# Kernel tuning notes

Hardware: AMD Instinct MI355X
Metric: run time of the kernel (lower is better)

The kernel has to match this reference:

```python
import jax, jax.numpy as jnp
import numpy as np

B, S, D_IN, H, BLOCKS, OUT_DIM = 32, 128, 16, 128, 3, 1
TAU = 0.5
BN_EPS = 1e-5


def _conv1d(x, w, b, dil):
    # x: [B, C, S], w: [O, I, K], 'same' padding with dilation (matches torch padding='same')
    y = jax.lax.conv_general_dilated(x, w, (1,), 'SAME', rhs_dilation=(dil,),
                                     dimension_numbers=('NCH', 'OIH', 'NCH'))
    return y + b[None, :, None]


def setup_inputs() -> dict:
    key = jax.random.key(0)
    ks = jax.random.split(key, 24)
    w = lambda k, shape, s=0.05: (jax.random.normal(k, shape, jnp.float32) * s)
    return {
        'data': jax.random.normal(ks[0], (B, S, D_IN), jnp.float32),
        'gumbel_u': jax.random.uniform(ks[1], (B, S * S, 2), jnp.float32),
        'w11': w(ks[2], (H, D_IN, 1)), 'b11': jnp.zeros((H,), jnp.float32),
        'w12': w(ks[3], (H, H, 3)),    'b12': jnp.zeros((H,), jnp.float32),
        'w21': w(ks[4], (H, D_IN, 1)), 'b21': jnp.zeros((H,), jnp.float32),
        'w22': w(ks[5], (H, H, 5)),    'b22': jnp.zeros((H,), jnp.float32),
        'w31': w(ks[6], (H, D_IN, 1)), 'b31': jnp.zeros((H,), jnp.float32),
        'wf': w(ks[7], (3 * H, H)),    'bf': jnp.zeros((H,), jnp.float32),
        'w1': w(ks[8], (2 * H, H)),    'b1': jnp.zeros((H,), jnp.float32),
        'w2': w(ks[9], (H, 2)),        'b2': jnp.zeros((2,), jnp.float32),
        'wl': w(ks[10], (BLOCKS, H, H)), 'bl': jnp.zeros((BLOCKS, H), jnp.float32),
        'wr': w(ks[11], (BLOCKS, H, H)),
        'gamma': jnp.ones((BLOCKS, H), jnp.float32), 'beta': jnp.zeros((BLOCKS, H), jnp.float32),
        'wg': w(ks[12], (BLOCKS, 1), 0.3), 'bg': jnp.zeros((1,), jnp.float32),
        'we': w(ks[13], (H, H // 2)),  'be': jnp.zeros((H // 2,), jnp.float32),
        'wo': w(ks[14], (H // 2, OUT_DIM)), 'bo': jnp.zeros((OUT_DIM,), jnp.float32),
    }


def reference(data, gumbel_u, w11, b11, w12, b12, w21, b21, w22, b22, w31, b31,
              wf, bf, w1, b1, w2, b2, wl, bl, wr, gamma, beta, wg, bg, we, be, wo, bo):
    b_, s_, _ = data.shape
    xd = jnp.transpose(data, (0, 2, 1))                    # [B, D_IN, S]
    # dilated TCN feature extraction
    x1 = _conv1d(_conv1d(xd, w11, b11, 1), w12, b12, 3)
    x2 = _conv1d(_conv1d(xd, w21, b21, 1), w22, b22, 5)
    x3 = _conv1d(xd, w31, b31, 1)
    x = jnp.concatenate([x1, x2, x3], axis=1)              # [B, 3H, S]
    x = jnp.transpose(x, (0, 2, 1))                        # [B, S, 3H]
    x = jax.nn.relu(x @ wf + bf)                           # [B, S, H] node features

    # edge scoring: pair (i,j) gets cat(sender=x[j], receiver=x[i]); fc1 split avoids [B,S,S,2H]
    hs = x @ w1[:H]                                        # sender part  [B, S, H]
    hr = x @ w1[H:]                                        # receiver part [B, S, H]
    h = jax.nn.relu(hs[:, None, :, :] + hr[:, :, None, :] + b1)  # [B, S(i), S(j), H]
    logits = h @ w2 + b2                                   # [B, S, S, 2]

    # hard gumbel-softmax, channel 0 = edge on
    u = jnp.clip(gumbel_u, 1e-6, 1.0 - 1e-6).reshape(b_, s_, s_, 2)
    g = -jnp.log(-jnp.log(u))
    y = (logits + g) / TAU
    adj = (jnp.argmax(y, axis=-1) == 0).astype(x.dtype)    # [B, S, S]
    # zero strict lower triangle (tri_mask) and diagonal (keep_self_loops=False)
    idx = jnp.arange(s_)
    adj = adj * (idx[None, :] > idx[:, None])[None]
    # edge_list in torch is non-differentiable -> no grad through adjacency
    adj = jax.lax.stop_gradient(adj)

    # SAGEConv (mean aggr) + BatchNorm, dense per-sample message passing
    deg = jnp.maximum(adj.sum(axis=1), 1.0)                # in-degree of target j, [B, S]
    xn = x
    outs = []
    for l in range(BLOCKS):
        agg = jnp.einsum('bij,bih->bjh', adj, xn) / deg[..., None]
        out = agg @ wl[l] + bl[l] + xn @ wr[l]             # lin_l(agg) + lin_r(x)
        m = out.mean(axis=(0, 1))
        v = out.var(axis=(0, 1))
        xn = (out - m) * jax.lax.rsqrt(v + BN_EPS) * gamma[l] + beta[l]
        outs.append(xn)

    stk = jnp.stack(outs, axis=-1)                          # [B, S, H, BLOCKS]
    xw = jax.nn.relu(jnp.einsum('bshk,ko->bsh', stk, wg) + bg[0])
    last = xw[:, -1]                                        # aggregate='last' -> [B, H]
    h2 = jax.nn.relu(last @ we + be)
    return h2 @ wo + bo                                     # [B, OUT_DIM]
```

## Files before the change

kernel.cpp:

```cpp
#include <hip/hip_runtime.h>
#include <math.h>

#define BB 32
#define SS 128
#define DIN 16
#define HH 128
#define NBSH (BB*SS*HH)

typedef __attribute__((ext_vector_type(8))) short short8;
typedef __attribute__((ext_vector_type(4))) float vf4;

__device__ __forceinline__ unsigned short f2bf(float x){
    union { float f; unsigned int u; } v; v.f = x;
    unsigned int r = v.u + 0x7FFF + ((v.u >> 16) & 1);
    return (unsigned short)(r >> 16);
}
__device__ __forceinline__ float bf2f(unsigned short b){
    union { unsigned int u; float f; } v; v.u = ((unsigned int)b) << 16;
    return v.f;
}

__global__ __launch_bounds__(256) void k_prep(
    const float* __restrict__ w12, const float* __restrict__ w22,
    const float* __restrict__ w31,
    const float* __restrict__ w11, const float* __restrict__ b11,
    const float* __restrict__ w21, const float* __restrict__ b21,
    const float* __restrict__ wl, const float* __restrict__ wr,
    const float* __restrict__ wf, const float* __restrict__ w1,
    float* __restrict__ W3, float* __restrict__ W5, float* __restrict__ W31T,
    float* __restrict__ Beff1, float* __restrict__ Beff2, float* __restrict__ accf,
    unsigned short* __restrict__ wHi, unsigned short* __restrict__ wLo,
    unsigned short* __restrict__ wfTH, unsigned short* __restrict__ wfTL,
    unsigned short* __restrict__ w1sTH, unsigned short* __restrict__ w1sTL,
    unsigned short* __restrict__ w1rTH, unsigned short* __restrict__ w1rTL)
{
    __shared__ float W12L[8*384];
    __shared__ float W22L[8*640];
    __shared__ float w11L[2048], w21L[2048], b11L[128], b21L[128];
    __shared__ float S[4096];
    int blk = blockIdx.x; int tid = threadIdx.x;

    if (blk < 16){
        int h0 = blk*8;
        for (int i = tid; i < 768; i += 256){
            int hl = i/96, o4 = i%96;
            *reinterpret_cast<float4*>(W12L + hl*384 + o4*4) =
                reinterpret_cast<const float4*>(w12)[(h0+hl)*96 + o4];
        }
        for (int i = tid; i < 1280; i += 256){
            int hl = i/160, o4 = i%160;
            *reinterpret_cast<float4*>(W22L + hl*640 + o4*4) =
                reinterpret_cast<const float4*>(w22)[(h0+hl)*160 + o4];
        }
        for (int i = tid; i < 512; i += 256)
            *reinterpret_cast<float4*>(w11L + i*4) = reinterpret_cast<const float4*>(w11)[i];
        for (int i = tid; i < 512; i += 256)
            *reinterpret_cast<float4*>(w21L + i*4) = reinterpret_cast<const float4*>(w21)[i];
        if (tid < 128){ b11L[tid] = b11[tid]; b21L[tid] = b21[tid]; }
        if (blk == 0){ for (int i = tid; i < 768; i += 256) accf[i] = 0.f; }
        __syncthreads();

        for (int T = tid; T < 1216; T += 256){
            if (T < 384){
                int hl = T/48, kd = T%48, k = kd>>4, d = kd&15;
                float a = 0.f;
                #pragma unroll 4
                for (int c = 0; c < HH; ++c) a = fmaf(W12L[hl*384 + c*3 + k], w11L[c*16 + d], a);
                W3[(k*16+d)*128 + h0+hl] = a;
            } else if (T < 1024){
                int tt = T-384, hl = tt/80, kd = tt%80, k = kd>>4, d = kd&15;
                float a = 0.f;
                #pragma unroll 4
                for (int c = 0; c < HH; ++c) a = fmaf(W22L[hl*640 + c*5 + k], w21L[c*16 + d], a);
                W5[(k*16+d)*128 + h0+hl] = a;
            } else if (T < 1048){
                int tt = T-1024, hl = tt/3, k = tt%3;
                float a = 0.f;
                #pragma unroll 4
                for (int c = 0; c < HH; ++c) a = fmaf(W12L[hl*384 + c*3 + k], b11L[c], a);
                Beff1[k*128 + h0+hl] = a;
            } else if (T < 1088){
                int tt = T-1048, hl = tt/5, k = tt%5;
                float a = 0.f;
                #pragma unroll 4
                for (int c = 0; c < HH; ++c) a = fmaf(W22L[hl*640 + c*5 + k], b21L[c], a);
                Beff2[k*128 + h0+hl] = a;
            } else {
                int tt = T-1088, hl = tt>>4, d = tt&15;
                W31T[d*128 + h0+hl] = w31[(h0+hl)*16 + d];
            }
        }
    } else if (blk < 40){
        int q = blk - 16;
        int h = tid & 127; int half = tid >> 7;
        for (int rl = half; rl < 32; rl += 2){
            int r = q*32 + rl;
            int m = r >> 7;
            int c = r & 127;
            const float* src = (m < 3) ? (wl + (size_t)m*16384) : (wr + (size_t)(m-3)*16384);
            float v = src[c*128 + h];
            unsigned short hi = f2bf(v);
            unsigned short lo = f2bf(v - bf2f(hi));
            wHi[(size_t)m*16384 + h*128 + c] = hi;
            wLo[(size_t)m*16384 + h*128 + c] = lo;
        }
    } else {
        int t2 = blk - 40;
        const float* src; unsigned short *dH, *dL; int kbase, rstride;
        if (t2 < 12){ src = wf + (size_t)t2*32*128; dH = wfTH; dL = wfTL; kbase = t2*32; rstride = 384; }
        else if (t2 < 16){ int c = t2-12; src = w1 + (size_t)c*32*128; dH = w1sTH; dL = w1sTL; kbase = c*32; rstride = 128; }
        else { int c = t2-16; src = w1 + 16384 + (size_t)c*32*128; dH = w1rTH; dL = w1rTL; kbase = c*32; rstride = 128; }
        for (int i = tid; i < 1024; i += 256)
            reinterpret_cast<float4*>(S)[i] = reinterpret_cast<const float4*>(src)[i];
        __syncthreads();
        for (int task = tid; task < 4096; task += 256){
            int h = task & 127, kl = task >> 7;
            float v = S[kl*128 + h];
            unsigned short hi = f2bf(v);
            dH[(size_t)h*rstride + kbase + kl] = hi;
            dL[(size_t)h*rstride + kbase + kl] = f2bf(v - bf2f(hi));
        }
    }
}

#define AHo 0
#define ALo 6272
#define xHo 12544
#define xLo 14720
__global__ __launch_bounds__(512) void k_fuse_all(
    const float* __restrict__ data,
    const float* __restrict__ W3, const float* __restrict__ W5,
    const float* __restrict__ W31T,
    const float* __restrict__ Beff1, const float* __restrict__ Beff2,
    const float* __restrict__ b12, const float* __restrict__ b22,
    const float* __restrict__ b31,
    const unsigned short* __restrict__ wfTH, const unsigned short* __restrict__ wfTL,
    const float* __restrict__ bf,
    const unsigned short* __restrict__ w1sTH, const unsigned short* __restrict__ w1sTL,
    const unsigned short* __restrict__ w1rTH, const unsigned short* __restrict__ w1rTL,
    const float* __restrict__ b1,
    float* __restrict__ hs, float* __restrict__ hrT, float* __restrict__ XT)
{
    __shared__ __align__(16) unsigned short pool[16896];
    __shared__ __align__(16) float dinT[16*40];
    __shared__ float bfL[128], b1L[128];
    int blk = blockIdx.x; int row0 = blk*16;
    int b = row0 >> 7; int s0 = row0 & 127;
    int tid = threadIdx.x; int lane = tid & 63; int w = tid >> 6;
    int h = tid & 127; int quarter = tid >> 7;
    int frow = lane & 15, fk = (lane >> 4) * 8;
    int ncol = w*16 + frow;

    for (int idx = tid; idx < 576; idx += 512){
        int r = idx >> 4, d = idx & 15;
        int sp = s0 - 10 + r;
        dinT[d*40 + r] = (sp >= 0 && sp < SS) ? data[(b*SS+sp)*DIN + d] : 0.f;
    }
    if (tid < 128){ bfL[tid] = bf[tid]; b1L[tid] = b1[tid]; }
    __syncthreads();

    float a1[4] = {0,0,0,0}, a2[4] = {0,0,0,0}, a3[4] = {0,0,0,0};
    int rb = quarter*4;
    for (int d = 0; d < DIN; ++d){
        float w3v[3], w5v[5];
        #pragma unroll
        for (int k = 0; k < 3; ++k) w3v[k] = W3[(k*DIN+d)*HH + h];
        #pragma unroll
        for (int k = 0; k < 5; ++k) w5v[k] = W5[(k*DIN+d)*HH + h];
        float w31v = W31T[d*HH + h];
        const float4* qp = reinterpret_cast<const float4*>(dinT + d*40 + rb);
        float4 q0=qp[0],q1=qp[1],q2=qp[2],q3=qp[3],q4=qp[4],q5=qp[5];
        float qf[24] = {q0.x,q0.y,q0.z,q0.w, q1.x,q1.y,q1.z,q1.w,
                        q2.x,q2.y,q2.z,q2.w, q3.x,q3.y,q3.z,q3.w,
                        q4.x,q4.y,q4.z,q4.w, q5.x,q5.y,q5.z,q5.w};
        #pragma unroll
        for (int tp = 0; tp < 4; ++tp){
            #pragma unroll
            for (int k = 0; k < 3; ++k) a1[tp] = fmaf(qf[tp+3*k+7], w3v[k], a1[tp]);
            #pragma unroll
            for (int k = 0; k < 5; ++k) a2[tp] = fmaf(qf[tp+5*k], w5v[k], a2[tp]);
            a3[tp] = fmaf(qf[tp+10], w31v, a3[tp]);
        }
    }
    {
        float be1[3] = {Beff1[h], Beff1[HH+h], Beff1[2*HH+h]};
        float be2[5] = {Beff2[h], Beff2[HH+h], Beff2[2*HH+h], Beff2[3*HH+h], Beff2[4*HH+h]};
        float bv12 = b12[h], bv22 = b22[h], bv31 = b31[h];
        #pragma unroll
        for (int tp = 0; tp < 4; ++tp){
            int rl = rb + tp;
            int s = s0 + rl;
            float v1 = a1[tp] + bv12;
            #pragma unroll
            for (int k = 0; k < 3; ++k)
                if ((unsigned)(s + 3*k - 3) < SS) v1 += be1[k];
            float v2 = a2[tp] + bv22;
            #pragma unroll
            for (int k = 0; k < 5; ++k)
                if ((unsigned)(s + 5*k - 10) < SS) v2 += be2[k];
            float v3 = a3[tp] + bv31;
            unsigned short h1 = f2bf(v1), h2 = f2bf(v2), h3 = f2bf(v3);
            pool[AHo + rl*392 + h]        = h1;
            pool[AHo + rl*392 + 128 + h]  = h2;
            pool[AHo + rl*392 + 256 + h]  = h3;
            pool[ALo + rl*392 + h]        = f2bf(v1 - bf2f(h1));
            pool[ALo + rl*392 + 128 + h]  = f2bf(v2 - bf2f(h2));
            pool[ALo + rl*392 + 256 + h]  = f2bf(v3 - bf2f(h3));
        }
    }
    __syncthreads();

    vf4 facc; facc = 0.f;
    const unsigned short* wfh = wfTH + (size_t)ncol*384 + fk;
    const unsigned short* wfl = wfTL + (size_t)ncol*384 + fk;
    for (int ch = 0; ch < 12; ++ch){
        int ck0 = ch*32;
        short8 ah = *reinterpret_cast<const short8*>(pool + AHo + frow*392 + ck0 + fk);
        short8 al = *reinterpret_cast<const short8*>(pool + ALo + frow*392 + ck0 + fk);
        short8 bh = *reinterpret_cast<const short8*>(wfh + ck0);
        short8 bl = *reinterpret_cast<const short8*>(wfl + ck0);
        facc = __builtin_amdgcn_mfma_f32_16x16x32_bf16(ah, bh, facc, 0,0,0);
        facc = __builtin_amdgcn_mfma_f32_16x16x32_bf16(ah, bl, facc, 0,0,0);
        facc = __builtin_amdgcn_mfma_f32_16x16x32_bf16(al, bh, facc, 0,0,0);
        facc = __builtin_amdgcn_mfma_f32_16x16x32_bf16(al, bl, facc, 0,0,0);
    }
    {
        float bfv = bfL[ncol];
        #pragma unroll
        for (int r = 0; r < 4; ++r){
            int m = (lane>>4)*4 + r;
            float v = fmaxf(facc[r] + bfv, 0.f);
            unsigned short hi = f2bf(v);
            pool[xHo + m*136 + ncol] = hi;
            pool[xLo + m*136 + ncol] = f2bf(v - bf2f(hi));
        }
    }
    __syncthreads();
    for (int task = tid; task < 2048; task += 512){
        int m = task & 15, c = task >> 4;
        float v = bf2f(pool[xHo + m*136 + c]) + bf2f(pool[xLo + m*136 + c]);
        XT[((size_t)(b*HH + c))*SS + s0 + m] = v;
    }

    vf4 as, ar; as = 0.f; ar = 0.f;
    for (int pass = 0; pass < 2; ++pass){
        const unsigned short* sH = (pass ? w1rTH : w1sTH) + (size_t)ncol*128 + fk;
        const unsigned short* sL = (pass ? w1rTL : w1sTL) + (size_t)ncol*128 + fk;
        vf4 acc; acc = 0.f;
        #pragma unroll
        for (int ch = 0; ch < 4; ++ch){
            int ck0 = ch*32;
            short8 ah = *reinterpret_cast<const short8*>(pool + xHo + frow*136 + ck0 + fk);
            short8 al = *reinterpret_cast<const short8*>(pool + xLo + frow*136 + ck0 + fk);
            short8 bh = *reinterpret_cast<const short8*>(sH + ck0);
            short8 bl = *reinterpret_cast<const short8*>(sL + ck0);
            acc = __builtin_amdgcn_mfma_f32_16x16x32_bf16(ah, bh, acc, 0,0,0);
            acc = __builtin_amdgcn_mfma_f32_16x16x32_bf16(ah, bl, acc, 0,0,0);
            acc = __builtin_amdgcn_mfma_f32_16x16x32_bf16(al, bh, acc, 0,0,0);
            acc = __builtin_amdgcn_mfma_f32_16x16x32_bf16(al, bl, acc, 0,0,0);
        }
        if (pass == 0) as = acc; else ar = acc;
    }
    {
        float b1v = b1L[ncol];
        #pragma unroll
        for (int r = 0; r < 4; ++r){
            int m = (lane>>4)*4 + r;
            hs[(size_t)(row0+m)*128 + ncol] = as[r];
            hrT[((size_t)(b*HH + ncol))*SS + s0 + m] = ar[r] + b1v;
        }
    }
}

__global__ __launch_bounds__(256) void k_adj(
    const float* __restrict__ hs, const float* __restrict__ hrT,
    const float* __restrict__ w2, const float* __restrict__ b2,
    const float* __restrict__ gu, unsigned short* __restrict__ adjT,
    float* __restrict__ deginv)
{
    int blk = blockIdx.x; int b = blk >> 4; int j0 = (blk & 15) * 8;
    int tid = threadIdx.x; int i = tid & 127; int g = tid >> 7;
    __shared__ float hsL[8][128];
    __shared__ float w20L[128], w21L[128];
    __shared__ int degS[8];
    for (int idx = tid; idx < 1024; idx += 256){
        int jj = idx >> 7, h = idx & 127;
        hsL[jj][h] = hs[(size_t)(b*SS + j0 + jj)*HH + h];
    }
    if (tid < 128){ w20L[tid] = w2[tid*2]; w21L[tid] = w2[tid*2+1]; }
    if (tid < 8) degS[tid] = 0;
    __syncthreads();
    float d0[4] = {0,0,0,0}, d1[4] = {0,0,0,0};
    const float* hrb = hrT + (size_t)b*HH*SS + i;
    #pragma unroll 4
    for (int h = 0; h < 128; ++h){
        float hrv = hrb[(size_t)h*SS];
        float wa = w20L[h], wb = w21L[h];
        float r0 = fmaxf(hsL[g*4+0][h] + hrv, 0.f);
        float r1 = fmaxf(hsL[g*4+1][h] + hrv, 0.f);
        float r2 = fmaxf(hsL[g*4+2][h] + hrv, 0.f);
        float r3 = fmaxf(hsL[g*4+3][h] + hrv, 0.f);
        d0[0]=fmaf(r0,wa,d0[0]); d1[0]=fmaf(r0,wb,d1[0]);
        d0[1]=fmaf(r1,wa,d0[1]); d1[1]=fmaf(r1,wb,d1[1]);
        d0[2]=fmaf(r2,wa,d0[2]); d1[2]=fmaf(r2,wb,d1[2]);
        d0[3]=fmaf(r3,wa,d0[3]); d1[3]=fmaf(r3,wb,d1[3]);
    }
    float b20 = b2[0], b21 = b2[1];
    #pragma unroll
    for (int jj = 0; jj < 4; ++jj){
        int j = j0 + g*4 + jj;
        size_t e = (size_t)(b*SS + i)*SS + j;
        float2 uv = *reinterpret_cast<const float2*>(gu + e*2);
        float u0 = fminf(fmaxf(uv.x, 1e-6f), 0.999999f);
        float u1 = fminf(fmaxf(uv.y, 1e-6f), 0.999999f);
        float g0 = -logf(-logf(u0));
        float g1 = -logf(-logf(u1));
        float y0 = d0[jj] + b20 + g0;
        float y1 = d1[jj] + b21 + g1;
        bool av = (j > i) && (y0 >= y1);
        adjT[(size_t)(b*SS + j)*SS + i] = av ? (unsigned short)0x3F80 : (unsigned short)0;
        unsigned long long msk = __ballot(av);
        if ((tid & 63) == 0) atomicAdd(&degS[g*4+jj], (int)__popcll(msk));
    }
    __syncthreads();
    if (tid < 8) deginv[b*SS + j0 + tid] = 1.f / fmaxf((float)degS[tid], 1.f);
}

#define AGGH 0
#define AGGL 4352
#define XH   8704
#define XL   17920
#define XNJH 27136
#define XNJL 31488
__global__ __launch_bounds__(512) void k_gnn(
    const unsigned short* __restrict__ adjT, const float* __restrict__ xnT,
    const float* __restrict__ deginv,
    const float* __restrict__ gammaP, const float* __restrict__ betaP,
    const float* __restrict__ accP, int aff,
    const unsigned short* __restrict__ wlH, const unsigned short* __restrict__ wlL,
    const unsigned short* __restrict__ wrH, const unsigned short* __restrict__ wrL,
    const float* __restrict__ bl,
    float* __restrict__ outT, float* __restrict__ accL)
{
    __shared__ __align__(16) unsigned short pool[35840];
    __shared__ float2 scsh[128];
    __shared__ float dinvL[32];
    __shared__ float2 redS[128];
    __shared__ float blL[128];
    int blk = blockIdx.x; int b = blk >> 2; int j0 = (blk & 3) * 32;
    int tid = threadIdx.x; int lane = tid & 63; int w = tid >> 6;
    int frow = lane & 15, fk = (lane >> 4) * 8;

    if (tid < 128){
        if (aff){
            float2 s = reinterpret_cast<const float2*>(accP)[tid];
            float m = s.x * (1.f/4096.f);
            float var = fmaxf(s.y * (1.f/4096.f) - m*m, 0.f);
            float sc = gammaP[tid] / sqrtf(var + 1e-5f);
            scsh[tid] = make_float2(sc, betaP[tid] - m*sc);
        } else scsh[tid] = make_float2(1.f, 0.f);
        redS[tid] = make_float2(0.f, 0.f);
        blL[tid] = bl[tid];
    }
    if (tid < 32) dinvL[tid] = deginv[b*SS + j0 + tid];
    __syncthreads();

    int mt = w & 1, ntb = (w >> 1) * 2;
    const unsigned short* adjrow = adjT + ((size_t)(b*SS + j0 + mt*16 + frow))*SS + fk;
    vf4 acc[2]; acc[0]=0.f; acc[1]=0.f;
    for (int cs = 0; cs < 2; ++cs){
        for (int task = tid; task < 2048; task += 512){
            int hh = task >> 4, q = task & 15;
            float4 v = *reinterpret_cast<const float4*>(
                xnT + ((size_t)(b*HH + hh))*SS + cs*64 + q*4);
            float2 ss = scsh[hh];
            float e0 = fmaf(v.x, ss.x, ss.y), e1 = fmaf(v.y, ss.x, ss.y);
            float e2 = fmaf(v.z, ss.x, ss.y), e3 = fmaf(v.w, ss.x, ss.y);
            unsigned short h0 = f2bf(e0), h1 = f2bf(e1), h2 = f2bf(e2), h3 = f2bf(e3);
            unsigned int hA = (unsigned int)h0 | ((unsigned int)h1 << 16);
            unsigned int hB = (unsigned int)h2 | ((unsigned int)h3 << 16);
            unsigned short l0 = f2bf(e0 - bf2f(h0)), l1 = f2bf(e1 - bf2f(h1));
            unsigned short l2 = f2bf(e2 - bf2f(h2)), l3 = f2bf(e3 - bf2f(h3));
            unsigned int lA = (unsigned int)l0 | ((unsigned int)l1 << 16);
            unsigned int lB = (unsigned int)l2 | ((unsigned int)l3 << 16);
            *reinterpret_cast<uint2*>(pool + XH + hh*72 + q*4) = make_uint2(hA, hB);
            *reinterpret_cast<uint2*>(pool + XL + hh*72 + q*4) = make_uint2(lA, lB);
        }
        __syncthreads();
        #pragma unroll
        for (int ks = 0; ks < 2; ++ks){
            short8 af = *reinterpret_cast<const short8*>(adjrow + cs*64 + ks*32);
            #pragma unroll
            for (int ntl = 0; ntl < 2; ++ntl){
                int nt = ntb + ntl;
                short8 bh = *reinterpret_cast<const short8*>(
                    pool + XH + (nt*16 + frow)*72 + ks*32 + fk);
                short8 bo = *reinterpret_cast<const short8*>(
                    pool + XL + (nt*16 + frow)*72 + ks*32 + fk);
                acc[ntl] = __builtin_amdgcn_mfma_f32_16x16x32_bf16(af, bh, acc[ntl], 0, 0, 0);
                acc[ntl] = __builtin_amdgcn_mfma_f32_16x16x32_bf16(af, bo, acc[ntl], 0, 0, 0);
            }
        }
        __syncthreads();
    }
    #pragma unroll
    for (int ntl = 0; ntl < 2; ++ntl){
        int hh = (ntb + ntl)*16 + frow;
        #pragma unroll
        for (int r = 0; r < 4; ++r){
            int jl = mt*16 + (lane>>4)*4 + r;
            float v = acc[ntl][r] * dinvL[jl];
            unsigned short hi = f2bf(v);
            pool[AGGH + jl*136 + hh] = hi;
            pool[AGGL + jl*136 + hh] = f2bf(v - bf2f(hi));
        }
    }
    if (tid < 256){
        int jg = tid >> 5, cg = tid & 31;
        float mv[4][4];
        #pragma unroll
        for (int e = 0; e < 4; ++e){
            float4 v = *reinterpret_cast<const float4*>(
                xnT + ((size_t)(b*HH + cg*4 + e))*SS + j0 + jg*4);
            float2 ss = scsh[cg*4 + e];
            mv[e][0]=fmaf(v.x,ss.x,ss.y); mv[e][1]=fmaf(v.y,ss.x,ss.y);
            mv[e][2]=fmaf(v.z,ss.x,ss.y); mv[e][3]=fmaf(v.w,ss.x,ss.y);
        }
        #pragma unroll
        for (int f = 0; f < 4; ++f){
            int jl = jg*4 + f;
            unsigned short h0=f2bf(mv[0][f]), h1=f2bf(mv[1][f]), h2=f2bf(mv[2][f]), h3=f2bf(mv[3][f]);
            unsigned int a0 = (unsigned int)h0 | ((unsigned int)h1<<16);
            unsigned int a1v = (unsigned int)h2 | ((unsigned int)h3<<16);
            unsigned short l0=f2bf(mv[0][f]-bf2f(h0)), l1=f2bf(mv[1][f]-bf2f(h1));
            unsigned short l2=f2bf(mv[2][f]-bf2f(h2)), l3=f2bf(mv[3][f]-bf2f(h3));
            unsigned int b0 = (unsigned int)l0 | ((unsigned int)l1<<16);
            unsigned int b1v = (unsigned int)l2 | ((unsigned int)l3<<16);
            *reinterpret_cast<uint2*>(pool + XNJH + jl*136 + cg*4) = make_uint2(a0, a1v);
            *reinterpret_cast<uint2*>(pool + XNJL + jl*136 + cg*4) = make_uint2(b0, b1v);
        }
    }
    __syncthreads();

    vf4 lacc[2]; lacc[0]=0.f; lacc[1]=0.f;
    int hh_a = w*16 + frow;
    const unsigned short* wlh = wlH + (size_t)hh_a*128 + fk;
    const unsigned short* wll = wlL + (size_t)hh_a*128 + fk;
    const unsigned short* wrh = wrH + (size_t)hh_a*128 + fk;
    const unsigned short* wrl = wrL + (size_t)hh_a*128 + fk;
    #pragma unroll
    for (int ck = 0; ck < 4; ++ck){
        int ck0 = ck*32;
        #pragma unroll
        for (int mat = 0; mat < 2; ++mat){
            short8 ah = *reinterpret_cast<const short8*>((mat ? wrh : wlh) + ck0);
            short8 al = *reinterpret_cast<const short8*>((mat ? wrl : wll) + ck0);
            int Bh = mat ? XNJH : AGGH;
            int Bl = mat ? XNJL : AGGL;
            #pragma unroll
            for (int ntl = 0; ntl < 2; ++ntl){
                short8 bh = *reinterpret_cast<const short8*>(
                    pool + Bh + (ntl*16 + frow)*136 + ck0 + fk);
                short8 bo = *reinterpret_cast<const short8*>(
                    pool + Bl + (ntl*16 + frow)*136 + ck0 + fk);
                lacc[ntl] = __builtin_amdgcn_mfma_f32_16x16x32_bf16(ah, bh, lacc[ntl], 0,0,0);
                lacc[ntl] = __builtin_amdgcn_mfma_f32_16x16x32_bf16(ah, bo, lacc[ntl], 0,0,0);
                lacc[ntl] = __builtin_amdgcn_mfma_f32_16x16x32_bf16(al, bh, lacc[ntl], 0,0,0);
            }
        }
    }
    #pragma unroll
    for (int ntl = 0; ntl < 2; ++ntl){
        #pragma unroll
        for (int r = 0; r < 4; ++r){
            int hh = w*16 + (lane>>4)*4 + r;
            int jl = ntl*16 + (lane & 15);
            float v = lacc[ntl][r] + blL[hh];
            outT[((size_t)(b*HH + hh))*SS + j0 + jl] = v;
            float s1 = v, s2 = v*v;
            #pragma unroll
            for (int off = 1; off < 16; off <<= 1){
                s1 += __shfl_xor(s1, off, 64);
                s2 += __shfl_xor(s2, off, 64);
            }
            if ((lane & 15) == 0){ redS[hh].x += s1; redS[hh].y += s2; }
        }
    }
    __syncthreads();
    if (tid < 128){
        atomicAdd(&accL[2*tid],   redS[tid].x);
        atomicAdd(&accL[2*tid+1], redS[tid].y);
    }
}

__global__ __launch_bounds__(128) void k_head(
    const float* __restrict__ t0, const float* __restrict__ t1,
    const float* __restrict__ t2, const float* __restrict__ accf,
    const float* __restrict__ gamma, const float* __restrict__ beta,
    const float* __restrict__ wg, const float* __restrict__ bg,
    const float* __restrict__ we, const float* __restrict__ be,
    const float* __restrict__ wo, const float* __restrict__ bo,
    float* __restrict__ out)
{
    int b = blockIdx.x; int t = threadIdx.x;
    __shared__ float xw[HH];
    const float* outs[3] = {t0, t1, t2};
    float a = bg[0];
    #pragma unroll
    for (int l = 0; l < 3; ++l){
        float2 s = reinterpret_cast<const float2*>(accf)[l*128 + t];
        float m = s.x * (1.f/4096.f);
        float var = fmaxf(s.y * (1.f/4096.f) - m*m, 0.f);
        float sc = gamma[l*128+t] / sqrtf(var + 1e-5f);
        float sh = beta[l*128+t] - m*sc;
        float val = fmaf(outs[l][((size_t)(b*HH + t))*SS + SS-1], sc, sh);
        a = fmaf(val, wg[l], a);
    }
    xw[t] = fmaxf(a, 0.f);
    __syncthreads();
    if (t < 64){
        float acc = be[t];
        for (int h = 0; h < HH; ++h) acc = fmaf(xw[h], we[h*64 + t], acc);
        float h2 = fmaxf(acc, 0.f);
        float r = h2 * wo[t];
        #pragma unroll
        for (int off = 32; off; off >>= 1) r += __shfl_down(r, off, 64);
        if (t == 0) out[b] = r + bo[0];
    }
}

extern "C" void kernel_launch(void* const* d_in, const int* in_sizes, int n_in,
                              void* d_out, int out_size, void* d_ws, size_t ws_size,
                              hipStream_t stream)
{
    const float* data = (const float*)d_in[0];
    const float* gu   = (const float*)d_in[1];
    const float* w11  = (const float*)d_in[2];
    const float* b11  = (const float*)d_in[3];
    const float* w12  = (const float*)d_in[4];
    const float* b12  = (const float*)d_in[5];
    const float* w21  = (const float*)d_in[6];
    const float* b21  = (const float*)d_in[7];
    const float* w22  = (const float*)d_in[8];
    const float* b22  = (const float*)d_in[9];
    const float* w31  = (const float*)d_in[10];
    const float* b31  = (const float*)d_in[11];
    const float* wf   = (const float*)d_in[12];
    const float* bf   = (const float*)d_in[13];
    const float* w1   = (const float*)d_in[14];
    const float* b1   = (const float*)d_in[15];
    const float* w2   = (const float*)d_in[16];
    const float* b2   = (const float*)d_in[17];
    const float* wl   = (const float*)d_in[18];
    const float* bl   = (const float*)d_in[19];
    const float* wr   = (const float*)d_in[20];
    const float* gamma= (const float*)d_in[21];
    const float* beta = (const float*)d_in[22];
    const float* wg   = (const float*)d_in[23];
    const float* bg   = (const float*)d_in[24];
    const float* we   = (const float*)d_in[25];
    const float* be   = (const float*)d_in[26];
    const float* wo   = (const float*)d_in[27];
    const float* bo   = (const float*)d_in[28];
    float* out = (float*)d_out;

    float* ws = (float*)d_ws;
    float* hs   = ws;
    float* hrT  = ws + (size_t)NBSH;
    float* XT   = ws + (size_t)2*NBSH;
    float* T0   = ws + (size_t)3*NBSH;
    float* T1   = ws + (size_t)4*NBSH;
    float* T2   = ws + (size_t)5*NBSH;
    float* G    = ws + (size_t)6*NBSH;
    float* W3    = G;
    float* W5    = G + 6144;
    float* W31T  = G + 16384;
    float* Beff1 = G + 18432;
    float* Beff2 = G + 18816;
    float* accf  = G + 19456;
    float* dinv  = G + 20224;
    unsigned short* adjTG = (unsigned short*)(G + 24320);
    unsigned short* wHi   = (unsigned short*)(G + 286464);
    unsigned short* wLo   = (unsigned short*)(G + 335616);
    unsigned short* wfTH  = (unsigned short*)(G + 384768);
    unsigned short* wfTL  = (unsigned short*)(G + 409344);
    unsigned short* w1sTH = (unsigned short*)(G + 433920);
    unsigned short* w1sTL = (unsigned short*)(G + 442112);
    unsigned short* w1rTH = (unsigned short*)(G + 450304);
    unsigned short* w1rTL = (unsigned short*)(G + 458496);

    k_prep<<<60, 256, 0, stream>>>(w12, w22, w31, w11, b11, w21, b21, wl, wr,
                                   wf, w1,
                                   W3, W5, W31T, Beff1, Beff2, accf, wHi, wLo,
                                   wfTH, wfTL, w1sTH, w1sTL, w1rTH, w1rTL);
    k_fuse_all<<<256, 512, 0, stream>>>(data, W3, W5, W31T, Beff1, Beff2,
                                        b12, b22, b31,
                                        wfTH, wfTL, bf, w1sTH, w1sTL, w1rTH, w1rTL, b1,
                                        hs, hrT, XT);
    k_adj<<<512, 256, 0, stream>>>(hs, hrT, w2, b2, gu, adjTG, dinv);

    const float* xnTs[3] = {XT, T0, T1};
    float*       outs[3] = {T0, T1, T2};
    for (int l = 0; l < 3; ++l){
        int aff = (l > 0);
        const float* gP = gamma + (l>0 ? (l-1)*HH : 0);
        const float* bP = beta  + (l>0 ? (l-1)*HH : 0);
        const float* aP = accf + (l>0 ? (l-1)*256 : 0);
        k_gnn<<<128, 512, 0, stream>>>(adjTG, xnTs[l], dinv, gP, bP, aP, aff,
            wHi + (size_t)l*16384, wLo + (size_t)l*16384,
            wHi + (size_t)(3+l)*16384, wLo + (size_t)(3+l)*16384,
            bl + (size_t)l*HH, outs[l], accf + (size_t)l*256);
    }
    k_head<<<BB, 128, 0, stream>>>(T0, T1, T2, accf, gamma, beta,
                                   wg, bg, we, be, wo, bo, out);
}
```

Before: 119.4 us.

## Split GNN layer kernel into 16-row target tiles across twice the blocks

Each k_gnn block now handles 16 target nodes instead of 32, so the grid doubles from 128 to 256 blocks and each wave computes one MFMA tile instead of two. Shared memory shrinks accordingly. This is meant to fill more compute units on the GPU, at the cost of each block re-staging the full per-sample xn tile (twice as much redundant global read and bf16 split work) and more atomics for the batch-norm statistics.

```diff
diff --git a/kernel.cpp b/kernel.cpp
--- a/kernel.cpp
+++ b/kernel.cpp
@@ -327,11 +327,11 @@
 }
 
 #define AGGH 0
-#define AGGL 4352
-#define XH   8704
-#define XL   17920
-#define XNJH 27136
-#define XNJL 31488
+#define AGGL 2176
+#define XH   4352
+#define XL   13568
+#define XNJH 22784
+#define XNJL 24960
 __global__ __launch_bounds__(512) void k_gnn(
     const unsigned short* __restrict__ adjT, const float* __restrict__ xnT,
     const float* __restrict__ deginv,
@@ -342,12 +342,12 @@
     const float* __restrict__ bl,
     float* __restrict__ outT, float* __restrict__ accL)
 {
-    __shared__ __align__(16) unsigned short pool[35840];
+    __shared__ __align__(16) unsigned short pool[27136];
     __shared__ float2 scsh[128];
-    __shared__ float dinvL[32];
+    __shared__ float dinvL[16];
     __shared__ float2 redS[128];
     __shared__ float blL[128];
-    int blk = blockIdx.x; int b = blk >> 2; int j0 = (blk & 3) * 32;
+    int blk = blockIdx.x; int b = blk >> 3; int j0 = (blk & 7) * 16;
     int tid = threadIdx.x; int lane = tid & 63; int w = tid >> 6;
     int frow = lane & 15, fk = (lane >> 4) * 8;
 
@@ -362,12 +362,11 @@
         redS[tid] = make_float2(0.f, 0.f);
         blL[tid] = bl[tid];
     }
-    if (tid < 32) dinvL[tid] = deginv[b*SS + j0 + tid];
-    __syncthreads();
-
-    int mt = w & 1, ntb = (w >> 1) * 2;
-    const unsigned short* adjrow = adjT + ((size_t)(b*SS + j0 + mt*16 + frow))*SS + fk;
-    vf4 acc[2]; acc[0]=0.f; acc[1]=0.f;
+    if (tid < 16) dinvL[tid] = deginv[b*SS + j0 + tid];
+    __syncthreads();
+
+    const unsigned short* adjrow = adjT + ((size_t)(b*SS + j0 + frow))*SS + fk;
+    vf4 acc; acc = 0.f;
     for (int cs = 0; cs < 2; ++cs){
         for (int task = tid; task < 2048; task += 512){
             int hh = task >> 4, q = task & 15;
@@ -390,32 +389,27 @@
         #pragma unroll
         for (int ks = 0; ks < 2; ++ks){
             short8 af = *reinterpret_cast<const short8*>(adjrow + cs*64 + ks*32);
-            #pragma unroll
-            for (int ntl = 0; ntl < 2; ++ntl){
-                int nt = ntb + ntl;
-                short8 bh = *reinterpret_cast<const short8*>(
-                    pool + XH + (nt*16 + frow)*72 + ks*32 + fk);
-                short8 bo = *reinterpret_cast<const short8*>(
-                    pool + XL + (nt*16 + frow)*72 + ks*32 + fk);
-                acc[ntl] = __builtin_amdgcn_mfma_f32_16x16x32_bf16(af, bh, acc[ntl], 0, 0, 0);
-                acc[ntl] = __builtin_amdgcn_mfma_f32_16x16x32_bf16(af, bo, acc[ntl], 0, 0, 0);
-            }
+            short8 bh = *reinterpret_cast<const short8*>(
+                pool + XH + (w*16 + frow)*72 + ks*32 + fk);
+            short8 bo = *reinterpret_cast<const short8*>(
+                pool + XL + (w*16 + frow)*72 + ks*32 + fk);
+            acc = __builtin_amdgcn_mfma_f32_16x16x32_bf16(af, bh, acc, 0, 0, 0);
+            acc = __builtin_amdgcn_mfma_f32_16x16x32_bf16(af, bo, acc, 0, 0, 0);
         }
         __syncthreads();
     }
-    #pragma unroll
-    for (int ntl = 0; ntl < 2; ++ntl){
-        int hh = (ntb + ntl)*16 + frow;
+    {
+        int hhc = w*16 + (lane & 15);
         #pragma unroll
         for (int r = 0; r < 4; ++r){
-            int jl = mt*16 + (lane>>4)*4 + r;
-            float v = acc[ntl][r] * dinvL[jl];
+            int jl = (lane>>4)*4 + r;
+            float v = acc[r] * dinvL[jl];
             unsigned short hi = f2bf(v);
-            pool[AGGH + jl*136 + hh] = hi;
-            pool[AGGL + jl*136 + hh] = f2bf(v - bf2f(hi));
-        }
-    }
-    if (tid < 256){
+            pool[AGGH + jl*136 + hhc] = hi;
+            pool[AGGL + jl*136 + hhc] = f2bf(v - bf2f(hi));
+        }
+    }
+    if (tid < 128){
         int jg = tid >> 5, cg = tid & 31;
         float mv[4][4];
         #pragma unroll
@@ -442,7 +436,7 @@
     }
     __syncthreads();
 
-    vf4 lacc[2]; lacc[0]=0.f; lacc[1]=0.f;
+    vf4 lacc; lacc = 0.f;
     int hh_a = w*16 + frow;
     const unsigned short* wlh = wlH + (size_t)hh_a*128 + fk;
     const unsigned short* wll = wlL + (size_t)hh_a*128 + fk;
@@ -457,34 +451,26 @@
             short8 al = *reinterpret_cast<const short8*>((mat ? wrl : wll) + ck0);
             int Bh = mat ? XNJH : AGGH;
             int Bl = mat ? XNJL : AGGL;
-            #pragma unroll
-            for (int ntl = 0; ntl < 2; ++ntl){
-                short8 bh = *reinterpret_cast<const short8*>(
-                    pool + Bh + (ntl*16 + frow)*136 + ck0 + fk);
-                short8 bo = *reinterpret_cast<const short8*>(
-                    pool + Bl + (ntl*16 + frow)*136 + ck0 + fk);
-                lacc[ntl] = __builtin_amdgcn_mfma_f32_16x16x32_bf16(ah, bh, lacc[ntl], 0,0,0);
-                lacc[ntl] = __builtin_amdgcn_mfma_f32_16x16x32_bf16(ah, bo, lacc[ntl], 0,0,0);
-                lacc[ntl] = __builtin_amdgcn_mfma_f32_16x16x32_bf16(al, bh, lacc[ntl], 0,0,0);
-            }
+            short8 bh = *reinterpret_cast<const short8*>(pool + Bh + frow*136 + ck0 + fk);
+            short8 bo = *reinterpret_cast<const short8*>(pool + Bl + frow*136 + ck0 + fk);
+            lacc = __builtin_amdgcn_mfma_f32_16x16x32_bf16(ah, bh, lacc, 0,0,0);
+            lacc = __builtin_amdgcn_mfma_f32_16x16x32_bf16(ah, bo, lacc, 0,0,0);
+            lacc = __builtin_amdgcn_mfma_f32_16x16x32_bf16(al, bh, lacc, 0,0,0);
         }
     }
     #pragma unroll
-    for (int ntl = 0; ntl < 2; ++ntl){
-        #pragma unroll
-        for (int r = 0; r < 4; ++r){
-            int hh = w*16 + (lane>>4)*4 + r;
-            int jl = ntl*16 + (lane & 15);
-            float v = lacc[ntl][r] + blL[hh];
-            outT[((size_t)(b*HH + hh))*SS + j0 + jl] = v;
-            float s1 = v, s2 = v*v;
-            #pragma unroll
-            for (int off = 1; off < 16; off <<= 1){
-                s1 += __shfl_xor(s1, off, 64);
-                s2 += __shfl_xor(s2, off, 64);
-            }
-            if ((lane & 15) == 0){ redS[hh].x += s1; redS[hh].y += s2; }
-        }
+    for (int r = 0; r < 4; ++r){
+        int hh = w*16 + (lane>>4)*4 + r;
+        int jl = lane & 15;
+        float v = lacc[r] + blL[hh];
+        outT[((size_t)(b*HH + hh))*SS + j0 + jl] = v;
+        float s1 = v, s2 = v*v;
+        #pragma unroll
+        for (int off = 1; off < 16; off <<= 1){
+            s1 += __shfl_xor(s1, off, 64);
+            s2 += __shfl_xor(s2, off, 64);
+        }
+        if ((lane & 15) == 0){ redS[hh].x += s1; redS[hh].y += s2; }
     }
     __syncthreads();
     if (tid < 128){
@@ -606,7 +592,7 @@
         const float* gP = gamma + (l>0 ? (l-1)*HH : 0);
         const float* bP = beta  + (l>0 ? (l-1)*HH : 0);
         const float* aP = accf + (l>0 ? (l-1)*256 : 0);
-        k_gnn<<<128, 512, 0, stream>>>(adjTG, xnTs[l], dinv, gP, bP, aP, aff,
+        k_gnn<<<256, 512, 0, stream>>>(adjTG, xnTs[l], dinv, gP, bP, aP, aff,
             wHi + (size_t)l*16384, wLo + (size_t)l*16384,
             wHi + (size_t)(3+l)*16384, wLo + (size_t)(3+l)*16384,
             bl + (size_t)l*HH, outs[l], accf + (size_t)l*256);
```

Measured after the change: 134.3 us. 1.13x slower.
